# Kernel optimization log

Hardware: AMD Instinct MI355X
Metric: run time of the kernel (lower is better)

## Reference

```python
import jax, jax.numpy as jnp
import numpy as np

N_BINS = 229
OUT_F = 88
MODEL = 128
W_SIZE = 30
WIN = 2 * W_SIZE + 1  # 61


def _window(spec):
    B, T, F = spec.shape
    padded = jnp.pad(spec, ((0, 0), (W_SIZE, W_SIZE), (0, 0)))
    idx = jnp.arange(T)[:, None] + jnp.arange(WIN)[None, :]
    return padded[:, idx, :]


def setup_inputs() -> dict:
    key = jax.random.key(0)
    ks = jax.random.split(key, 12)
    B, T = 4, 1024
    s = 0.05
    return {
        "spec": jax.random.normal(ks[0], (B, T, N_BINS), dtype=jnp.float32),
        # frame_stack: Linear(N_BINS -> OUT_F)
        "W_frame": jax.random.normal(ks[1], (N_BINS, OUT_F), dtype=jnp.float32) * s,
        "b_frame": jnp.zeros((OUT_F,), dtype=jnp.float32),
        # onset attention: Linear(N_BINS + N_BINS -> MODEL), v: Linear(MODEL -> 1, no bias)
        "W_attn_o": jax.random.normal(ks[2], (2 * N_BINS, MODEL), dtype=jnp.float32) * s,
        "b_attn_o": jnp.zeros((MODEL,), dtype=jnp.float32),
        "v_o": jax.random.normal(ks[3], (MODEL,), dtype=jnp.float32) * s,
        # onset linear1: Linear(N_BINS -> OUT_F)
        "W_lin1": jax.random.normal(ks[4], (N_BINS, OUT_F), dtype=jnp.float32) * s,
        "b_lin1": jnp.zeros((OUT_F,), dtype=jnp.float32),
        # combine attention: Linear(2*OUT_F + N_BINS -> MODEL)
        "W_attn_c": jax.random.normal(ks[5], (2 * OUT_F + N_BINS, MODEL), dtype=jnp.float32) * s,
        "b_attn_c": jnp.zeros((MODEL,), dtype=jnp.float32),
        "v_c": jax.random.normal(ks[6], (MODEL,), dtype=jnp.float32) * s,
        # combine linear: Linear(2*OUT_F + N_BINS -> OUT_F)
        "W_linc": jax.random.normal(ks[7], (2 * OUT_F + N_BINS, OUT_F), dtype=jnp.float32) * s,
        "b_linc": jnp.zeros((OUT_F,), dtype=jnp.float32),
    }


def _attend(hidden, win, Wa, ba, v):
    B, T, Wn, F = win.shape
    h = jnp.broadcast_to(hidden[:, :, None, :], (B, T, Wn, hidden.shape[-1]))
    energy = jnp.tanh(jnp.concatenate([h, win], axis=-1) @ Wa + ba)
    scores = energy @ v
    return jax.nn.softmax(scores, axis=-1)


def reference(spec, W_frame, b_frame, W_attn_o, b_attn_o, v_o, W_lin1, b_lin1,
              W_attn_c, b_attn_c, v_c, W_linc, b_linc):
    win = _window(spec)

    feat_pred = spec @ W_frame + b_frame  # [B,T,OUT_F]

    # Onset stack
    a_onset = _attend(spec, win, W_attn_o, b_attn_o, v_o)
    weighted_o = jnp.einsum('btw,btwf->btf', a_onset, win)  # [B,T,N_BINS]
    onset_pred = jax.nn.sigmoid(weighted_o @ W_lin1 + b_lin1)  # [B,T,OUT_F]

    # Combine stack
    x = jnp.concatenate([feat_pred, onset_pred], axis=-1)  # [B,T,2*OUT_F]
    a_frame = _attend(x, win, W_attn_c, b_attn_c, v_c)
    weighted_c = jnp.einsum('btw,btwf->btf', a_frame, win)  # [B,T,N_BINS]
    frame_pred = jax.nn.sigmoid(jnp.concatenate([x, weighted_c], axis=-1) @ W_linc + b_linc)

    return (frame_pred, a_frame[:, :, None, :], onset_pred, a_onset[:, :, None, :], feat_pred)
```

## Files before the change

kernel.cpp:

```cpp
#include <hip/hip_runtime.h>

#define NBINS 229
#define OUTF  88
#define MODEL 128
#define WSZ   30
#define WIN   61
#define TLEN  1024
#define BT    4096

#define NC1 648
#define NP1 704
#define NC2 216

typedef short bf16x8 __attribute__((ext_vector_type(8)));
typedef float f32x4 __attribute__((ext_vector_type(4)));
typedef unsigned short ushort_t;

__device__ __forceinline__ float sigmoid_f(float x) {
    return __builtin_amdgcn_rcpf(1.f + __expf(-x));
}
__device__ __forceinline__ ushort_t f2bf(float f) {
    unsigned u = __float_as_uint(f);
    return (ushort_t)((u + 0x7fffu + ((u >> 16) & 1u)) >> 16);
}

__device__ __forceinline__ float dot8(uint4 pv, float4 ha, float4 hb,
                                      float4 va, float4 vb) {
    float r;
    r  = va.x * __builtin_amdgcn_rcpf(__builtin_fmaf(ha.x, __uint_as_float(pv.x << 16), 1.f));
    r += va.y * __builtin_amdgcn_rcpf(__builtin_fmaf(ha.y, __uint_as_float(pv.x & 0xffff0000u), 1.f));
    r += va.z * __builtin_amdgcn_rcpf(__builtin_fmaf(ha.z, __uint_as_float(pv.y << 16), 1.f));
    r += va.w * __builtin_amdgcn_rcpf(__builtin_fmaf(ha.w, __uint_as_float(pv.y & 0xffff0000u), 1.f));
    r += vb.x * __builtin_amdgcn_rcpf(__builtin_fmaf(hb.x, __uint_as_float(pv.z << 16), 1.f));
    r += vb.y * __builtin_amdgcn_rcpf(__builtin_fmaf(hb.y, __uint_as_float(pv.z & 0xffff0000u), 1.f));
    r += vb.z * __builtin_amdgcn_rcpf(__builtin_fmaf(hb.z, __uint_as_float(pv.w << 16), 1.f));
    r += vb.w * __builtin_amdgcn_rcpf(__builtin_fmaf(hb.w, __uint_as_float(pv.w & 0xffff0000u), 1.f));
    return r;
}

__device__ __forceinline__ bf16x8 cvt8(f32x4 a, f32x4 b) {
    bf16x8 r;
    r[0] = (short)f2bf(a.x); r[1] = (short)f2bf(a.y);
    r[2] = (short)f2bf(a.z); r[3] = (short)f2bf(a.w);
    r[4] = (short)f2bf(b.x); r[5] = (short)f2bf(b.y);
    r[6] = (short)f2bf(b.z); r[7] = (short)f2bf(b.w);
    return r;
}
__device__ __forceinline__ bf16x8 loadA(const float* sp, int k0) {
    if (k0 > 228) return (bf16x8)(short)0;
    f32x4 a, b;
    __builtin_memcpy(&a, sp + k0, 16);
    if (k0 <= 216) {
        __builtin_memcpy(&b, sp + k0 + 4, 16);
    } else {
        b = (f32x4){sp[228], 0.f, 0.f, 0.f};
    }
    return cvt8(a, b);
}

#define GP_BLOCKS 897

__global__ __launch_bounds__(256) void gemm_prep(
    const float* __restrict__ spec,
    const float* __restrict__ Wf,  const float* __restrict__ bfr,
    const float* __restrict__ Wao, const float* __restrict__ bao,
    const float* __restrict__ Wl1,
    const float* __restrict__ Wac, const float* __restrict__ bac,
    const float* __restrict__ Wlc,
    const float* __restrict__ vo,  const float* __restrict__ vc,
    float* __restrict__ feat, float* __restrict__ EHo_,
    ushort_t* __restrict__ EPo_, ushort_t* __restrict__ EPc_,
    ushort_t* __restrict__ Rb_,  ushort_t* __restrict__ Qb_,
    ushort_t* __restrict__ B2b, float* __restrict__ bias2,
    float* __restrict__ sv)
{
    __shared__ ushort_t B1t[64 * 256];
    __shared__ float red[4];
    const int tid = threadIdx.x;
    const int b = blockIdx.x;

    if (b < 704) {
        const int e = b & 7, kf = b >> 3;
        const int rb = (e * 8 + (kf & 7)) * 64;
        const int cb = (kf >> 3) * 64;

        {
            const int n  = tid & 63;
            const int kq = tid >> 6;
            const int ng = cb + n;
            const float* srcp = nullptr; int sstr = 0;
            if (ng < 88)       { srcp = Wf  + ng;                          sstr = 88;  }
            else if (ng < 216) { srcp = Wao + (ng - 88);                   sstr = 128; }
            else if (ng < 344) { srcp = Wao + (size_t)NBINS * 128 + (ng - 216); sstr = 128; }
            else if (ng < 472) { srcp = Wac + (size_t)176 * 128 + (ng - 344);   sstr = 128; }
            else if (ng < 560) { srcp = Wl1 + (ng - 472);                  sstr = 88;  }
            else if (ng < NC1) { srcp = Wlc + (size_t)176 * 88 + (ng - 560);    sstr = 88; }
            const int n31 = n & 31;
#pragma unroll
            for (int it = 0; it < 8; it++) {
                const int k8 = kq * 8 + it * 32;
                bf16x8 vv;
#pragma unroll
                for (int j = 0; j < 8; j++) {
                    const int k = k8 + j;
                    float v = (srcp && k < NBINS) ? srcp[(size_t)k * sstr] : 0.f;
                    vv[j] = (short)f2bf(v);
                }
                const int chunk = (kq + 4 * it) ^ n31;
                *(bf16x8*)&B1t[n * 256 + chunk * 8] = vv;
            }
        }
        __syncthreads();

        const int wv = tid >> 6, ln = tid & 63;
        const int l15 = ln & 15, qd = ln >> 4;
        const float* sp = spec + (size_t)(rb + wv * 16 + l15) * NBINS;

        f32x4 acc[4];
#pragma unroll
        for (int nt = 0; nt < 4; nt++) acc[nt] = (f32x4){0.f, 0.f, 0.f, 0.f};

        bf16x8 af = loadA(sp, qd * 8);
#pragma unroll
        for (int it = 0; it < 8; it++) {
            const int nk = (it + 1 < 8) ? (it + 1) * 32 : 0;
            bf16x8 an = loadA(sp, nk + qd * 8);
            const int cq = qd + 4 * it;
#pragma unroll
            for (int nt = 0; nt < 4; nt++) {
                const int nn = nt * 16 + l15;
                bf16x8 bv = *(const bf16x8*)&B1t[nn * 256 + ((cq ^ (nn & 31)) << 3)];
                acc[nt] = __builtin_amdgcn_mfma_f32_16x16x32_bf16(
                    af, bv, acc[nt], 0, 0, 0);
            }
            af = an;
        }

        const int mbase = rb + wv * 16 + qd * 4;
#pragma unroll
        for (int nt = 0; nt < 4; nt++) {
            const int n = cb + nt * 16 + l15;
            if (n < NC1) {
                const float bn = (n < 88) ? bfr[n] : (n < 216 ? bao[n - 88] : 0.f);
#pragma unroll
                for (int r = 0; r < 4; r++) {
                    const int m = mbase + r;
                    float val = acc[nt][r] + bn;
                    if (n < 88) {
                        feat[(size_t)m * 88 + n] = val;
                    } else if (n < 216) {
                        EHo_[(size_t)m * 128 + (n - 88)] = __expf(val + val);
                    } else if (n < 344) {
                        EPo_[(size_t)m * 128 + (n - 216)] = f2bf(__expf(val + val));
                    } else if (n < 472) {
                        EPc_[(size_t)m * 128 + (n - 344)] = f2bf(__expf(val + val));
                    } else if (n < 560) {
                        Rb_[(size_t)m * 96 + (n - 472)] = f2bf(val);
                    } else {
                        Qb_[(size_t)m * 96 + (n - 560)] = f2bf(val);
                    }
                }
            }
        }
    } else if (b < 896) {
        int idx = (b - 704) * 256 + tid;
        int n = idx / 192, k = idx - n * 192;
        float v = 0.f;
        if (k < 176 && n < NC2)
            v = (n < 128) ? Wac[k * MODEL + n] : Wlc[k * 88 + (n - 128)];
        B2b[idx] = f2bf(v);
    } else {
        bias2[tid] = (tid < 128) ? bac[tid] : 0.f;
        int wid = tid >> 6, lane = tid & 63;
        const float* vp = (wid < 2) ? vo : vc;
        float val = vp[(wid & 1) * 64 + lane];
#pragma unroll
        for (int m = 32; m; m >>= 1) val += __shfl_xor(val, m, 64);
        if (lane == 0) red[wid] = val;
        __syncthreads();
        if (tid == 0) {
            sv[0] = red[0] + red[1];
            sv[1] = red[2] + red[3];
        }
    }
}

#define EPST 136
#define RST  96
#define XST  200
#define AST  104

#define PLO_O 0
#define RL_O  (68 * EPST)
#define PLC_O (RL_O + 68 * RST)
#define QL_O  (PLC_O + 68 * EPST)
#define XB_O  (QL_O + 68 * RST)
#define AM_O  (XB_O + 16 * XST)
#define EHC_O (AM_O + 16 * AST)
#define BSC_O (EHC_O + 2048)
#define SH_U16 ((BSC_O + 1408))

__global__ __launch_bounds__(512) void attn_fused(
    const float* __restrict__ EHo,
    const ushort_t* __restrict__ EPo_g,
    const ushort_t* __restrict__ Rb,
    const ushort_t* __restrict__ EPc_g,
    const ushort_t* __restrict__ Qb,
    const float* __restrict__ feat,
    const ushort_t* __restrict__ B2b,
    const float* __restrict__ bias2,
    const float* __restrict__ vo, const float* __restrict__ vc,
    const float* __restrict__ svp,
    const float* __restrict__ bl1, const float* __restrict__ blc,
    float* __restrict__ a_o_out, float* __restrict__ onset_out,
    float* __restrict__ a_c_out, float* __restrict__ frame_out)
{
    __shared__ alignas(16) ushort_t SH[SH_U16];
    ushort_t* Plo = SH + PLO_O;
    ushort_t* Rl  = SH + RL_O;
    ushort_t* Plc = SH + PLC_O;
    ushort_t* Ql  = SH + QL_O;
    ushort_t* Xb  = SH + XB_O;
    ushort_t* Am  = SH + AM_O;
    float*    EHc   = (float*)(SH + EHC_O);
    float*    basec = (float*)(SH + BSC_O);

    const int tid = threadIdx.x;
    const int s0 = ((blockIdx.x & 7) * 64 + (blockIdx.x >> 3)) * 8;
    const int t0 = s0 & (TLEN - 1);

    for (int i = tid; i < 68 * 16; i += 512) {
        int j = i >> 4, c = (i & 15) * 8;
        int cs = ((i & 15) ^ ((j >> 3) & 7)) * 8;
        int tg = t0 + j - WSZ;
        uint4 vP = {0x3f803f80u, 0x3f803f80u, 0x3f803f80u, 0x3f803f80u};
        uint4 vC = vP;
        if ((unsigned)tg < (unsigned)TLEN) {
            vP = *(const uint4*)&EPo_g[(size_t)(s0 - WSZ + j) * 128 + c];
            vC = *(const uint4*)&EPc_g[(size_t)(s0 - WSZ + j) * 128 + c];
        }
        *(uint4*)&Plo[j * EPST + cs] = vP;
        *(uint4*)&Plc[j * EPST + cs] = vC;
    }
    for (int i = tid; i < 68; i += 512) {
        *(uint4*)&Plo[i * EPST + 128] = (uint4){0u, 0u, 0u, 0u};
        *(uint4*)&Plc[i * EPST + 128] = (uint4){0u, 0u, 0u, 0u};
    }
    for (int i = tid; i < 68 * 12; i += 512) {
        int j = i / 12, c = (i - j * 12) * 8;
        int tg = t0 + j - WSZ;
        uint4 vR = {0u, 0u, 0u, 0u}, vQ = {0u, 0u, 0u, 0u};
        if ((unsigned)tg < (unsigned)TLEN) {
            vR = *(const uint4*)&Rb[(size_t)(s0 - WSZ + j) * 96 + c];
            vQ = *(const uint4*)&Qb[(size_t)(s0 - WSZ + j) * 96 + c];
        }
        *(uint4*)&Rl[j * RST + c] = vR;
        *(uint4*)&Ql[j * RST + c] = vQ;
    }
    for (int i = tid; i < 16 * XST; i += 512) {
        int r = i / XST, k = i - r * XST;
        ushort_t v = 0;
        if (r < 8 && k < 88) v = f2bf(feat[(size_t)(s0 + r) * 88 + k]);
        Xb[i] = v;
    }
    {
        unsigned* am32 = (unsigned*)Am;
        for (int i = tid; i < 16 * 48; i += 512)
            am32[(i / 48) * 52 + (i % 48)] = 0u;
    }
    __syncthreads();

    const int q = tid >> 6;
    const int w = tid & 63;
    const int s = s0 + q;
    const int su = __builtin_amdgcn_readfirstlane(s);
    const int row = q + ((w < WIN) ? w : 0);
    const int rsw = (row >> 3) & 7;
    const int l15 = w & 15, qd = w >> 4;

    {
        const ushort_t* pb = &Plo[row * EPST];
        const float* hrow = EHo + (size_t)su * 128;
        float accr = 0.f;
#pragma unroll
        for (int d8 = 0; d8 < 16; d8++) {
            uint4 pv = *(const uint4*)(pb + ((d8 ^ rsw) << 3));
            float4 ha = *(const float4*)(hrow + d8 * 8);
            float4 hb = *(const float4*)(hrow + d8 * 8 + 4);
            float4 va = *(const float4*)(vo + d8 * 8);
            float4 vb = *(const float4*)(vo + d8 * 8 + 4);
            accr += dot8(pv, ha, hb, va, vb);
        }
        float eng = svp[0] - 2.f * accr;
        float ex = (w < WIN) ? __expf(eng) : 0.f;
        float sm = ex;
#pragma unroll
        for (int m = 32; m; m >>= 1) sm += __shfl_xor(sm, m, 64);
        float a = ex * __builtin_amdgcn_rcpf(sm);
        if (w < WIN) {
            a_o_out[(size_t)s * WIN + w] = a;
            Am[q * AST + q + w] = f2bf(a);
        }
    }
    __syncthreads();

    if (q < 6) {
        f32x4 acc = (f32x4){0.f, 0.f, 0.f, 0.f};
#pragma unroll
        for (int kk = 0; kk < 3; kk++) {
            bf16x8 av = *(const bf16x8*)&Am[l15 * AST + kk * 32 + qd * 8];
            bf16x8 bv;
#pragma unroll
            for (int j = 0; j < 8; j++)
                bv[j] = (short)Rl[(kk * 32 + qd * 8 + j) * RST + q * 16 + l15];
            acc = __builtin_amdgcn_mfma_f32_16x16x32_bf16(av, bv, acc, 0, 0, 0);
        }
        const int f = q * 16 + l15;
        if (qd < 2 && f < 88) {
            const float bb = bl1[f];
#pragma unroll
            for (int r = 0; r < 4; r++) {
                const int m = qd * 4 + r;
                float p = sigmoid_f(acc[r] + bb);
                onset_out[(size_t)(s0 + m) * OUTF + f] = p;
                Xb[m * XST + 88 + f] = f2bf(p);
            }
        }
    }
    __syncthreads();

    {
#pragma unroll
        for (int rt = 0; rt < 2; rt++) {
            const int t = q + rt * 8;
            if (t < 14) {
                const int n0 = t * 16;
                const ushort_t* bp = B2b + (size_t)(n0 + l15) * 192 + qd * 8;
                const ushort_t* ap = &Xb[l15 * XST + qd * 8];
                f32x4 acc = (f32x4){0.f, 0.f, 0.f, 0.f};
#pragma unroll
                for (int it = 0; it < 6; it++) {
                    bf16x8 av = *(const bf16x8*)(ap + it * 32);
                    bf16x8 bv = *(const bf16x8*)(bp + it * 32);
                    acc = __builtin_amdgcn_mfma_f32_16x16x32_bf16(
                        av, bv, acc, 0, 0, 0);
                }
                if (qd < 2) {
                    const int n = n0 + l15;
                    const float b2 = bias2[n];
#pragma unroll
                    for (int r = 0; r < 4; r++) {
                        const int m = qd * 4 + r;
                        float val = acc[r] + b2;
                        if (n < 128)        EHc[m * 128 + n] = __expf(val + val);
                        else if (n < NC2)   basec[m * 88 + (n - 128)] = val;
                    }
                }
            }
        }
    }
    __syncthreads();

    {
        const ushort_t* pb = &Plc[row * EPST];
        const float* hl = &EHc[q * 128];
        float accr = 0.f;
#pragma unroll
        for (int d8 = 0; d8 < 16; d8++) {
            uint4 pv = *(const uint4*)(pb + ((d8 ^ rsw) << 3));
            float4 ha = *(const float4*)(hl + d8 * 8);
            float4 hb = *(const float4*)(hl + d8 * 8 + 4);
            float4 va = *(const float4*)(vc + d8 * 8);
            float4 vb = *(const float4*)(vc + d8 * 8 + 4);
            accr += dot8(pv, ha, hb, va, vb);
        }
        float eng = svp[1] - 2.f * accr;
        float ex = (w < WIN) ? __expf(eng) : 0.f;
        float sm = ex;
#pragma unroll
        for (int m = 32; m; m >>= 1) sm += __shfl_xor(sm, m, 64);
        float a = ex * __builtin_amdgcn_rcpf(sm);
        if (w < WIN) {
            a_c_out[(size_t)s * WIN + w] = a;
            Am[q * AST + q + w] = f2bf(a);
        }
    }
    __syncthreads();

    if (q < 6) {
        f32x4 acc = (f32x4){0.f, 0.f, 0.f, 0.f};
#pragma unroll
        for (int kk = 0; kk < 3; kk++) {
            bf16x8 av = *(const bf16x8*)&Am[l15 * AST + kk * 32 + qd * 8];
            bf16x8 bv;
#pragma unroll
            for (int j = 0; j < 8; j++)
                bv[j] = (short)Ql[(kk * 32 + qd * 8 + j) * RST + q * 16 + l15];
            acc = __builtin_amdgcn_mfma_f32_16x16x32_bf16(av, bv, acc, 0, 0, 0);
        }
        const int f = q * 16 + l15;
        if (qd < 2 && f < 88) {
            const float bb = blc[f];
#pragma unroll
            for (int r = 0; r < 4; r++) {
                const int m = qd * 4 + r;
                float p = sigmoid_f(acc[r] + bb + basec[m * 88 + f]);
                frame_out[(size_t)(s0 + m) * OUTF + f] = p;
            }
        }
    }
}

extern "C" void kernel_launch(void* const* d_in, const int* in_sizes, int n_in,
                              void* d_out, int out_size, void* d_ws, size_t ws_size,
                              hipStream_t stream)
{
    const float* spec = (const float*)d_in[0];
    const float* Wf   = (const float*)d_in[1];
    const float* bf_  = (const float*)d_in[2];
    const float* Wao  = (const float*)d_in[3];
    const float* bao  = (const float*)d_in[4];
    const float* vo   = (const float*)d_in[5];
    const float* Wl1  = (const float*)d_in[6];
    const float* bl1  = (const float*)d_in[7];
    const float* Wac  = (const float*)d_in[8];
    const float* bac  = (const float*)d_in[9];
    const float* vc   = (const float*)d_in[10];
    const float* Wlc  = (const float*)d_in[11];
    const float* blc  = (const float*)d_in[12];

    float* out  = (float*)d_out;
    float* out0 = out;
    float* out1 = out + 360448;
    float* out2 = out + 610304;
    float* out3 = out + 970752;
    float* out4 = out + 1220608;

    float* ws = (float*)d_ws;
    float*    sv    = ws;
    float*    bias2 = ws + 16;
    ushort_t* B2b   = (ushort_t*)(ws + 272);
    float*    EHo   = ws + 24848;
    ushort_t* EPo   = (ushort_t*)(ws + 549136);
    ushort_t* EPc   = (ushort_t*)(ws + 811280);
    ushort_t* Rb    = (ushort_t*)(ws + 1073424);
    ushort_t* Qb    = (ushort_t*)(ws + 1270032);
    (void)ws_size; (void)in_sizes; (void)n_in; (void)out_size;

    gemm_prep<<<GP_BLOCKS, 256, 0, stream>>>(
        spec, Wf, bf_, Wao, bao, Wl1, Wac, bac, Wlc, vo, vc,
        out4, EHo, EPo, EPc, Rb, Qb, B2b, bias2, sv);

    attn_fused<<<BT / 8, 512, 0, stream>>>(
        EHo, EPo, Rb, EPc, Qb, out4, B2b, bias2, vo, vc, sv, bl1, blc,
        out3, out2, out1, out0);
}
```

Before: 111.9 us.

## Share LDS buffers between onset and combine stages and pack dot math into float2

The onset and combine stages now share one set of shared-memory buffers for the windowed projections and value rows. The combine-stage data is loaded after the onset stage finishes instead of up front, which roughly halves LDS use. Launch bounds now request more resident blocks per CU, and the attention dot product uses two-wide float vectors so the compiler can emit packed FMA/MUL instructions. The cost is an extra barrier and a global load that can no longer overlap with the onset work, plus register pressure from the tighter launch bound.

New measurement: 112.0 us. About the same (+0.1%).

```diff
diff --git a/kernel.cpp b/kernel.cpp
--- a/kernel.cpp
+++ b/kernel.cpp
@@ -14,6 +14,7 @@
 
 typedef short bf16x8 __attribute__((ext_vector_type(8)));
 typedef float f32x4 __attribute__((ext_vector_type(4)));
+typedef float f32x2 __attribute__((ext_vector_type(2)));
 typedef unsigned short ushort_t;
 
 __device__ __forceinline__ float sigmoid_f(float x) {
@@ -24,18 +25,27 @@
     return (ushort_t)((u + 0x7fffu + ((u >> 16) & 1u)) >> 16);
 }
 
-__device__ __forceinline__ float dot8(uint4 pv, float4 ha, float4 hb,
-                                      float4 va, float4 vb) {
-    float r;
-    r  = va.x * __builtin_amdgcn_rcpf(__builtin_fmaf(ha.x, __uint_as_float(pv.x << 16), 1.f));
-    r += va.y * __builtin_amdgcn_rcpf(__builtin_fmaf(ha.y, __uint_as_float(pv.x & 0xffff0000u), 1.f));
-    r += va.z * __builtin_amdgcn_rcpf(__builtin_fmaf(ha.z, __uint_as_float(pv.y << 16), 1.f));
-    r += va.w * __builtin_amdgcn_rcpf(__builtin_fmaf(ha.w, __uint_as_float(pv.y & 0xffff0000u), 1.f));
-    r += vb.x * __builtin_amdgcn_rcpf(__builtin_fmaf(hb.x, __uint_as_float(pv.z << 16), 1.f));
-    r += vb.y * __builtin_amdgcn_rcpf(__builtin_fmaf(hb.y, __uint_as_float(pv.z & 0xffff0000u), 1.f));
-    r += vb.z * __builtin_amdgcn_rcpf(__builtin_fmaf(hb.z, __uint_as_float(pv.w << 16), 1.f));
-    r += vb.w * __builtin_amdgcn_rcpf(__builtin_fmaf(hb.w, __uint_as_float(pv.w & 0xffff0000u), 1.f));
-    return r;
+__device__ __forceinline__ f32x2 dot8v(uint4 pv, float4 ha, float4 hb,
+                                       float4 va, float4 vb, f32x2 acc) {
+    const f32x2 one = {1.f, 1.f};
+    f32x2 p, x, r;
+    p = (f32x2){__uint_as_float(pv.x << 16), __uint_as_float(pv.x & 0xffff0000u)};
+    x = (f32x2){ha.x, ha.y} * p + one;
+    r = (f32x2){__builtin_amdgcn_rcpf(x.x), __builtin_amdgcn_rcpf(x.y)};
+    acc = (f32x2){va.x, va.y} * r + acc;
+    p = (f32x2){__uint_as_float(pv.y << 16), __uint_as_float(pv.y & 0xffff0000u)};
+    x = (f32x2){ha.z, ha.w} * p + one;
+    r = (f32x2){__builtin_amdgcn_rcpf(x.x), __builtin_amdgcn_rcpf(x.y)};
+    acc = (f32x2){va.z, va.w} * r + acc;
+    p = (f32x2){__uint_as_float(pv.z << 16), __uint_as_float(pv.z & 0xffff0000u)};
+    x = (f32x2){hb.x, hb.y} * p + one;
+    r = (f32x2){__builtin_amdgcn_rcpf(x.x), __builtin_amdgcn_rcpf(x.y)};
+    acc = (f32x2){vb.x, vb.y} * r + acc;
+    p = (f32x2){__uint_as_float(pv.w << 16), __uint_as_float(pv.w & 0xffff0000u)};
+    x = (f32x2){hb.z, hb.w} * p + one;
+    r = (f32x2){__builtin_amdgcn_rcpf(x.x), __builtin_amdgcn_rcpf(x.y)};
+    acc = (f32x2){vb.z, vb.w} * r + acc;
+    return acc;
 }
 
 __device__ __forceinline__ bf16x8 cvt8(f32x4 a, f32x4 b) {
@@ -185,22 +195,21 @@
     }
 }
 
+#define ROWS 68
 #define EPST 136
 #define RST  96
 #define XST  200
 #define AST  104
 
-#define PLO_O 0
-#define RL_O  (68 * EPST)
-#define PLC_O (RL_O + 68 * RST)
-#define QL_O  (PLC_O + 68 * EPST)
-#define XB_O  (QL_O + 68 * RST)
+#define PB_O  0
+#define RB_O  (ROWS * EPST)
+#define XB_O  (RB_O + ROWS * RST)
 #define AM_O  (XB_O + 16 * XST)
 #define EHC_O (AM_O + 16 * AST)
-#define BSC_O (EHC_O + 2048)
-#define SH_U16 ((BSC_O + 1408))
-
-__global__ __launch_bounds__(512) void attn_fused(
+#define BSC_O (EHC_O + 2 * 8 * 128)
+#define SH_U16 (BSC_O + 2 * 8 * 88)
+
+__global__ __launch_bounds__(512, 6) void attn_fused(
     const float* __restrict__ EHo,
     const ushort_t* __restrict__ EPo_g,
     const ushort_t* __restrict__ Rb,
@@ -216,12 +225,10 @@
     float* __restrict__ a_c_out, float* __restrict__ frame_out)
 {
     __shared__ alignas(16) ushort_t SH[SH_U16];
-    ushort_t* Plo = SH + PLO_O;
-    ushort_t* Rl  = SH + RL_O;
-    ushort_t* Plc = SH + PLC_O;
-    ushort_t* Ql  = SH + QL_O;
-    ushort_t* Xb  = SH + XB_O;
-    ushort_t* Am  = SH + AM_O;
+    ushort_t* Pbuf = SH + PB_O;
+    ushort_t* Rbuf = SH + RB_O;
+    ushort_t* Xb   = SH + XB_O;
+    ushort_t* Am   = SH + AM_O;
     float*    EHc   = (float*)(SH + EHC_O);
     float*    basec = (float*)(SH + BSC_O);
 
@@ -229,33 +236,22 @@
     const int s0 = ((blockIdx.x & 7) * 64 + (blockIdx.x >> 3)) * 8;
     const int t0 = s0 & (TLEN - 1);
 
-    for (int i = tid; i < 68 * 16; i += 512) {
+    for (int i = tid; i < ROWS * 16; i += 512) {
         int j = i >> 4, c = (i & 15) * 8;
         int cs = ((i & 15) ^ ((j >> 3) & 7)) * 8;
         int tg = t0 + j - WSZ;
         uint4 vP = {0x3f803f80u, 0x3f803f80u, 0x3f803f80u, 0x3f803f80u};
-        uint4 vC = vP;
-        if ((unsigned)tg < (unsigned)TLEN) {
+        if ((unsigned)tg < (unsigned)TLEN)
             vP = *(const uint4*)&EPo_g[(size_t)(s0 - WSZ + j) * 128 + c];
-            vC = *(const uint4*)&EPc_g[(size_t)(s0 - WSZ + j) * 128 + c];
-        }
-        *(uint4*)&Plo[j * EPST + cs] = vP;
-        *(uint4*)&Plc[j * EPST + cs] = vC;
-    }
-    for (int i = tid; i < 68; i += 512) {
-        *(uint4*)&Plo[i * EPST + 128] = (uint4){0u, 0u, 0u, 0u};
-        *(uint4*)&Plc[i * EPST + 128] = (uint4){0u, 0u, 0u, 0u};
-    }
-    for (int i = tid; i < 68 * 12; i += 512) {
+        *(uint4*)&Pbuf[j * EPST + cs] = vP;
+    }
+    for (int i = tid; i < ROWS * 12; i += 512) {
         int j = i / 12, c = (i - j * 12) * 8;
         int tg = t0 + j - WSZ;
-        uint4 vR = {0u, 0u, 0u, 0u}, vQ = {0u, 0u, 0u, 0u};
-        if ((unsigned)tg < (unsigned)TLEN) {
+        uint4 vR = {0u, 0u, 0u, 0u};
+        if ((unsigned)tg < (unsigned)TLEN)
             vR = *(const uint4*)&Rb[(size_t)(s0 - WSZ + j) * 96 + c];
-            vQ = *(const uint4*)&Qb[(size_t)(s0 - WSZ + j) * 96 + c];
-        }
-        *(uint4*)&Rl[j * RST + c] = vR;
-        *(uint4*)&Ql[j * RST + c] = vQ;
+        *(uint4*)&Rbuf[j * RST + c] = vR;
     }
     for (int i = tid; i < 16 * XST; i += 512) {
         int r = i / XST, k = i - r * XST;
@@ -279,9 +275,9 @@
     const int l15 = w & 15, qd = w >> 4;
 
     {
-        const ushort_t* pb = &Plo[row * EPST];
+        const ushort_t* pb = &Pbuf[row * EPST];
         const float* hrow = EHo + (size_t)su * 128;
-        float accr = 0.f;
+        f32x2 acc2 = {0.f, 0.f};
 #pragma unroll
         for (int d8 = 0; d8 < 16; d8++) {
             uint4 pv = *(const uint4*)(pb + ((d8 ^ rsw) << 3));
@@ -289,9 +285,9 @@
             float4 hb = *(const float4*)(hrow + d8 * 8 + 4);
             float4 va = *(const float4*)(vo + d8 * 8);
             float4 vb = *(const float4*)(vo + d8 * 8 + 4);
-            accr += dot8(pv, ha, hb, va, vb);
-        }
-        float eng = svp[0] - 2.f * accr;
+            acc2 = dot8v(pv, ha, hb, va, vb, acc2);
+        }
+        float eng = svp[0] - 2.f * (acc2.x + acc2.y);
         float ex = (w < WIN) ? __expf(eng) : 0.f;
         float sm = ex;
 #pragma unroll
@@ -312,7 +308,7 @@
             bf16x8 bv;
 #pragma unroll
             for (int j = 0; j < 8; j++)
-                bv[j] = (short)Rl[(kk * 32 + qd * 8 + j) * RST + q * 16 + l15];
+                bv[j] = (short)Rbuf[(kk * 32 + qd * 8 + j) * RST + q * 16 + l15];
             acc = __builtin_amdgcn_mfma_f32_16x16x32_bf16(av, bv, acc, 0, 0, 0);
         }
         const int f = q * 16 + l15;
@@ -361,10 +357,29 @@
     }
     __syncthreads();
 
+    for (int i = tid; i < ROWS * 16; i += 512) {
+        int j = i >> 4, c = (i & 15) * 8;
+        int cs = ((i & 15) ^ ((j >> 3) & 7)) * 8;
+        int tg = t0 + j - WSZ;
+        uint4 vC = {0x3f803f80u, 0x3f803f80u, 0x3f803f80u, 0x3f803f80u};
+        if ((unsigned)tg < (unsigned)TLEN)
+            vC = *(const uint4*)&EPc_g[(size_t)(s0 - WSZ + j) * 128 + c];
+        *(uint4*)&Pbuf[j * EPST + cs] = vC;
+    }
+    for (int i = tid; i < ROWS * 12; i += 512) {
+        int j = i / 12, c = (i - j * 12) * 8;
+        int tg = t0 + j - WSZ;
+        uint4 vQ = {0u, 0u, 0u, 0u};
+        if ((unsigned)tg < (unsigned)TLEN)
+            vQ = *(const uint4*)&Qb[(size_t)(s0 - WSZ + j) * 96 + c];
+        *(uint4*)&Rbuf[j * RST + c] = vQ;
+    }
+    __syncthreads();
+
     {
-        const ushort_t* pb = &Plc[row * EPST];
+        const ushort_t* pb = &Pbuf[row * EPST];
         const float* hl = &EHc[q * 128];
-        float accr = 0.f;
+        f32x2 acc2 = {0.f, 0.f};
 #pragma unroll
         for (int d8 = 0; d8 < 16; d8++) {
             uint4 pv = *(const uint4*)(pb + ((d8 ^ rsw) << 3));
@@ -372,9 +387,9 @@
             float4 hb = *(const float4*)(hl + d8 * 8 + 4);
             float4 va = *(const float4*)(vc + d8 * 8);
             float4 vb = *(const float4*)(vc + d8 * 8 + 4);
-            accr += dot8(pv, ha, hb, va, vb);
-        }
-        float eng = svp[1] - 2.f * accr;
+            acc2 = dot8v(pv, ha, hb, va, vb, acc2);
+        }
+        float eng = svp[1] - 2.f * (acc2.x + acc2.y);
         float ex = (w < WIN) ? __expf(eng) : 0.f;
         float sm = ex;
 #pragma unroll
@@ -395,7 +410,7 @@
             bf16x8 bv;
 #pragma unroll
             for (int j = 0; j < 8; j++)
-                bv[j] = (short)Ql[(kk * 32 + qd * 8 + j) * RST + q * 16 + l15];
+                bv[j] = (short)Rbuf[(kk * 32 + qd * 8 + j) * RST + q * 16 + l15];
             acc = __builtin_amdgcn_mfma_f32_16x16x32_bf16(av, bv, acc, 0, 0, 0);
         }
         const int f = q * 16 + l15;
```
